# Kernel optimization log

Hardware: AMD Instinct MI355X
Metric: run time of the kernel (lower is better)

Reference implementation:

```python
import jax, jax.numpy as jnp
import numpy as np

K = 5          # kernel_size per dim
B = 100        # batch size (hard-coded in source)
GRID = 28
NUM_FIRST_FC = 49  # adjs[2].size(0) = 7*7


def spline_conv(x, edge_index, pseudo, W, root, bias):
    """Degree-1 open B-spline graph conv (SplineGCN).
    x: [N, Cin]; edge_index: [2, E] (src, dst); pseudo: [E, 2] in [0,1];
    W: [K*K, Cin, Cout]; root: [Cin, Cout]; bias: [Cout].
    out_i = mean_{j->i} sum_taps b_tap(u_ij) * (x_j @ W[k_tap]) + x_i @ root + bias
    """
    N = x.shape[0]
    src, dst = edge_index[0], edge_index[1]
    pos = pseudo * (K - 1)                     # open spline: scale to [0, K-1]
    kf = jnp.floor(pos)
    frac = pos - kf                            # [E, 2]
    k0 = kf.astype(jnp.int32)
    k1 = jnp.minimum(k0 + 1, K - 1)
    # Precompute x @ W[k] for all 25 kernel indices: [N, K*K, Cout]
    y = jnp.einsum('ni,kio->nko', x, W)
    fx, fy = frac[:, 0], frac[:, 1]
    taps = [
        (k0[:, 0], k0[:, 1], (1 - fx) * (1 - fy)),
        (k0[:, 0], k1[:, 1], (1 - fx) * fy),
        (k1[:, 0], k0[:, 1], fx * (1 - fy)),
        (k1[:, 0], k1[:, 1], fx * fy),
    ]
    msg = jnp.zeros((src.shape[0], W.shape[2]), dtype=x.dtype)
    for ax, ay, w in taps:
        msg = msg + w[:, None] * y[src, ax * K + ay]   # gather [E, Cout]
    agg = jax.ops.segment_sum(msg, dst, num_segments=N)
    deg = jax.ops.segment_sum(jnp.ones_like(msg[:, 0]), dst, num_segments=N)
    return agg / jnp.maximum(deg, 1.0)[:, None] + x @ root + bias


def max_pool2(x):  # x: [b, H, W, C] -> [b, H/2, W/2, C] (same math as NCHW pool)
    b, h, w, c = x.shape
    return x.reshape(b, h // 2, 2, w // 2, 2, c).max(axis=(2, 4))


def setup_inputs() -> dict:
    key = jax.random.key(0)
    ks = jax.random.split(key, 16)
    N0, N1 = B * GRID * GRID, B * (GRID // 2) * (GRID // 2)
    E0, E1 = N0 * 8, N1 * 8
    s = 0.1
    return {
        'x': jax.random.normal(ks[0], (N0, 1), dtype=jnp.float32),
        'pseudo0': jax.random.uniform(ks[1], (E0, 2), dtype=jnp.float32),
        'pseudo1': jax.random.uniform(ks[2], (E1, 2), dtype=jnp.float32),
        'W1': jax.random.normal(ks[3], (K * K, 1, 32), dtype=jnp.float32) * s,
        'root1': jax.random.normal(ks[4], (1, 32), dtype=jnp.float32) * s,
        'b1': jnp.zeros((32,), dtype=jnp.float32),
        'W2': jax.random.normal(ks[5], (K * K, 32, 64), dtype=jnp.float32) * s,
        'root2': jax.random.normal(ks[6], (32, 64), dtype=jnp.float32) * s,
        'b2': jnp.zeros((64,), dtype=jnp.float32),
        'fc1_w': jax.random.normal(ks[7], (NUM_FIRST_FC * 64, 512), dtype=jnp.float32) * 0.02,
        'fc1_b': jnp.zeros((512,), dtype=jnp.float32),
        'fc2_w': jax.random.normal(ks[8], (512, 10), dtype=jnp.float32) * 0.02,
        'fc2_b': jnp.zeros((10,), dtype=jnp.float32),
        'edge_index0': jax.random.randint(ks[9], (2, E0), 0, N0, dtype=jnp.int32),
        'edge_index1': jax.random.randint(ks[10], (2, E1), 0, N1, dtype=jnp.int32),
    }


def reference(x, pseudo0, pseudo1, W1, root1, b1, W2, root2, b2,
              fc1_w, fc1_b, fc2_w, fc2_b, edge_index0, edge_index1):
    elu = jax.nn.elu
    # conv1 on 28x28 grid graph
    h = elu(spline_conv(x, edge_index0, pseudo0, W1, root1, b1))   # [B*784, 32]
    h = h.reshape(-1, GRID, GRID, 32)                              # [B, 28, 28, 32]
    h = max_pool2(h)                                               # [B, 14, 14, 32]
    h = h.reshape(-1, 32)                                          # [B*196, 32]
    # conv2 on 14x14 grid graph
    h = elu(spline_conv(h, edge_index1, pseudo1, W2, root2, b2))   # [B*196, 64]
    # faithful replication of the source's reshapes: (B*196) rows -> (B/4, 28, 28, 64)
    h = h.reshape(-1, GRID, GRID, 64)                              # [25, 28, 28, 64]
    h = max_pool2(h)                                               # [25, 14, 14, 64]
    h = h.reshape(-1, NUM_FIRST_FC * 64)                           # [100, 3136]
    h = elu(h @ fc1_w + fc1_b)
    # F.dropout with training=False (eval) is identity
    h = elu(h @ fc2_w + fc2_b)
    return jax.nn.log_softmax(h, axis=-1)
```

## Files before the change

kernel.cpp:

```cpp
#include <hip/hip_runtime.h>
#include <hip/hip_bf16.h>

#define KK 5
constexpr int N0 = 78400;
constexpr int E0 = 627200;
constexpr int N1 = 19600;
constexpr int E1 = 156800;
constexpr int C1 = 32, C2 = 64;
constexpr int BSZ = 100;
constexpr int FC1_IN = 3136, FC1_OUT = 512;
constexpr int NKEYS = 98000;
constexpr int NCOARSE = 383;
constexpr int CAPB = 2400;
constexpr int KEXT = 832;
constexpr int ULS = 836;
constexpr int UBS = 856;
constexpr int CH2 = 160;

typedef __attribute__((ext_vector_type(8))) short bf16x8;
typedef __attribute__((ext_vector_type(4))) float f32x4;

__device__ __forceinline__ unsigned short f2bf(float f) {
    union { float f; unsigned u; } v; v.f = f;
    unsigned u = v.u;
    unsigned r = (u + 0x7FFF + ((u >> 16) & 1)) >> 16;
    return (unsigned short)r;
}

__device__ __forceinline__ void taps4(float px, float py,
                                      int& a00, int& a01, int& a10, int& a11,
                                      float& fx, float& fy) {
    float kfx = floorf(px), kfy = floorf(py);
    fx = px - kfx; fy = py - kfy;
    int k0x = min(max((int)kfx, 0), KK - 1);
    int k0y = min(max((int)kfy, 0), KK - 1);
    int k1x = min(k0x + 1, KK - 1), k1y = min(k0y + 1, KK - 1);
    a00 = k0x * KK + k0y; a01 = k0x * KK + k1y;
    a10 = k1x * KK + k0y; a11 = k1x * KK + k1y;
}

__global__ void coarse_bin(const int* __restrict__ ei0, const int* __restrict__ ei1,
                           int* __restrict__ gcur, int* __restrict__ pk) {
    __shared__ int hist[NCOARSE];
    __shared__ int gbase[NCOARSE];
    int t = threadIdx.x;
    for (int i = t; i < NCOARSE; i += 512) hist[i] = 0;
    __syncthreads();
    int e0b = blockIdx.x * 4096;
    int ids[8], keys[8], rnk[8];
#pragma unroll
    for (int j = 0; j < 8; j++) {
        int e = e0b + t + j * 512;
        int gk = -1, id = 0;
        if (e < E0) { gk = ei0[E0 + e]; id = e; }
        else if (e < E0 + E1) { int el = e - E0; gk = N0 + ei1[E1 + el]; id = el; }
        ids[j] = id; keys[j] = gk;
    }
#pragma unroll
    for (int j = 0; j < 8; j++)
        if (keys[j] >= 0) rnk[j] = atomicAdd(&hist[keys[j] >> 8], 1);
    __syncthreads();
    for (int i = t; i < NCOARSE; i += 512)
        gbase[i] = hist[i] ? atomicAdd(&gcur[i], hist[i]) : 0;
    __syncthreads();
#pragma unroll
    for (int j = 0; j < 8; j++) {
        if (keys[j] >= 0) {
            int b = keys[j] >> 8;
            int p = gbase[b] + rnk[j];
            if (p < CAPB) pk[b * CAPB + p] = ids[j] | ((keys[j] & 255) << 20);
        }
    }
}

__global__ void tiny_scan(const int* __restrict__ gcur, int* __restrict__ db,
                          int* __restrict__ off) {
    __shared__ int tmp[NCOARSE];
    int t = threadIdx.x;
    if (t < NCOARSE) tmp[t] = min(gcur[t], CAPB);
    __syncthreads();
    if (t == 0) {
        int s = 0;
        for (int i = 0; i < NCOARSE; i++) { int c = tmp[i]; tmp[i] = s; s += c; }
    }
    __syncthreads();
    if (t < NCOARSE) db[t] = tmp[t];
    if (t == 0) off[NKEYS] = E0 + E1;
}

__global__ void fine_sort(const int* __restrict__ pk, const int* __restrict__ gcur,
                          const int* __restrict__ db,
                          int* __restrict__ idxx, int* __restrict__ off) {
    __shared__ int ent[CAPB];
    __shared__ int rnk[CAPB];
    __shared__ int h2[256];
    __shared__ int sc[256];
    int b = blockIdx.x, t = threadIdx.x;
    int cb = min(gcur[b], CAPB);
    int base = db[b];
    h2[t] = 0;
    __syncthreads();
    for (int i = t; i < cb; i += 256) {
        int v = pk[b * CAPB + i];
        ent[i] = v;
        rnk[i] = atomicAdd(&h2[(v >> 20) & 255], 1);
    }
    __syncthreads();
    int v0 = h2[t];
    sc[t] = v0;
    __syncthreads();
    for (int d = 1; d < 256; d <<= 1) {
        int add = (t >= d) ? sc[t - d] : 0;
        __syncthreads();
        sc[t] += add;
        __syncthreads();
    }
    int excl = sc[t] - v0;
    __syncthreads();
    sc[t] = excl;
    __syncthreads();
    int n = (b << 8) + t;
    if (n < NKEYS) off[n] = base + excl;
    for (int i = t; i < cb; i += 256) {
        int v = ent[i];
        idxx[base + sc[(v >> 20) & 255] + rnk[i]] = v & 0xFFFFF;
    }
}

__global__ __launch_bounds__(256, 5)
void conv1_fused(const int* __restrict__ idxx, const int* __restrict__ off,
                 const float* __restrict__ x, const int* __restrict__ ei0,
                 const float* __restrict__ ps0, const float* __restrict__ W1,
                 const float* __restrict__ root, const float* __restrict__ bias,
                 float* __restrict__ h1) {
    __shared__ float S4[256 * 25];
    __shared__ float Sr[64 * 25];
    int t = threadIdx.x;
    int nb = blockIdx.x * 64;
    int q = t & 3, nl = t >> 2;
    int n = nb + nl;
    float* sp = S4 + t * 25;
#pragma unroll
    for (int a = 0; a < 25; a++) sp[a] = 0.f;
    int e0 = off[n], e1 = off[n + 1];
    for (int p = e0 + q; p < e1; p += 4) {
        int e = idxx[p];
        int src = ei0[e];
        int a00, a01, a10, a11; float fx, fy;
        taps4(ps0[2 * e] * (KK - 1), ps0[2 * e + 1] * (KK - 1),
              a00, a01, a10, a11, fx, fy);
        float xv = x[src];
        float gx = 1.f - fx, gy = 1.f - fy;
        sp[a00] += gx * gy * xv; sp[a01] += gx * fy * xv;
        sp[a10] += fx * gy * xv; sp[a11] += fx * fy * xv;
    }
    __syncthreads();
    for (int idx2 = t; idx2 < 64 * 25; idx2 += 256) {
        int n2 = idx2 / 25, a = idx2 - n2 * 25;
        Sr[idx2] = S4[(n2 * 4 + 0) * 25 + a] + S4[(n2 * 4 + 1) * 25 + a] +
                   S4[(n2 * 4 + 2) * 25 + a] + S4[(n2 * 4 + 3) * 25 + a];
    }
    __syncthreads();
    int o = t & 31, ng = t >> 5;
    float w1c[25];
#pragma unroll
    for (int a = 0; a < 25; a++) w1c[a] = W1[a * C1 + o];
    float ro = root[o], bo = bias[o];
    for (int j = 0; j < 8; j++) {
        int nl2 = ng * 8 + j;
        int n2 = nb + nl2;
        float acc = 0.f;
#pragma unroll
        for (int a = 0; a < 25; a++) acc += Sr[nl2 * 25 + a] * w1c[a];
        float invd = 1.f / fmaxf((float)(off[n2 + 1] - off[n2]), 1.f);
        float v = acc * invd + x[n2] * ro + bo;
        h1[n2 * C1 + o] = v > 0.f ? v : expm1f(v);
    }
}

__global__ void pool1(const float* __restrict__ h1, float* __restrict__ p1) {
    int idx = blockIdx.x * blockDim.x + threadIdx.x;
    if (idx >= N1 * C1) return;
    int o = idx & 31; int t = idx >> 5;
    int c = t % 14; int r = (t / 14) % 14; int b = t / 196;
    const float* base = h1 + (((b * 28 + 2 * r) * 28 + 2 * c) * C1 + o);
    float m = fmaxf(fmaxf(base[0], base[C1]),
                    fmaxf(base[28 * C1], base[28 * C1 + C1]));
    p1[idx] = m;
}

__global__ void w2t_prep(const float* __restrict__ W2, const float* __restrict__ root2,
                         unsigned short* __restrict__ w2t) {
    int idx = blockIdx.x * blockDim.x + threadIdx.x;
    if (idx >= 64 * KEXT) return;
    int o = idx / KEXT, k = idx - o * KEXT;
    float v = (k < 800) ? W2[k * 64 + o] : root2[(k - 800) * 64 + o];
    w2t[idx] = f2bf(v);
}

__global__ void wt1_prep(const float* __restrict__ w, unsigned short* __restrict__ wt1) {
    __shared__ unsigned short tile[64 * 66];
    int t = threadIdx.x;
    int k0 = blockIdx.x * 64, j0 = blockIdx.y * 64;
    int jj = t & 63, ks = t >> 6;
    for (int kk = ks; kk < 64; kk += 4)
        tile[kk * 66 + jj] = f2bf(w[(k0 + kk) * FC1_OUT + j0 + jj]);
    __syncthreads();
    int kk = t & 63, js = t >> 6;
    for (int j2 = js; j2 < 64; j2 += 4)
        wt1[(j0 + j2) * FC1_IN + k0 + kk] = tile[kk * 66 + j2];
}

__global__ __launch_bounds__(256, 5)
void conv2_fused(const float* __restrict__ p1, const int* __restrict__ idxx,
                 const int* __restrict__ off, const int* __restrict__ ei1,
                 const float* __restrict__ ps1,
                 const unsigned short* __restrict__ w2t,
                 const float* __restrict__ b2, float* __restrict__ h2) {
    __shared__ float Ul[8 * ULS];
    __shared__ int   es[CH2];
    __shared__ int   et[CH2];
    __shared__ float efx[CH2], efy[CH2];
    unsigned short* Ub = (unsigned short*)Ul;
    int t = threadIdx.x;
    int nb = blockIdx.x * 8;
    int i = t & 31, g = t >> 5;
    float* up = Ul + g * ULS;
#pragma unroll
    for (int a = 0; a < 25; a++) up[a * 32 + i] = 0.f;
    up[800 + i] = p1[(nb + g) * C1 + i];
    int e0 = off[N0 + nb], e1 = off[N0 + nb + 8];
    int my0 = off[N0 + nb + g], my1 = off[N0 + nb + g + 1];
    for (int base = e0; base < e1; base += CH2) {
        int nE = min(e1 - base, CH2);
        __syncthreads();
        for (int j = t; j < nE; j += 256) {
            int e = idxx[base + j];
            es[j] = ei1[e];
            int a00, a01, a10, a11; float fx, fy;
            taps4(ps1[2 * e] * (KK - 1), ps1[2 * e + 1] * (KK - 1),
                  a00, a01, a10, a11, fx, fy);
            et[j] = a00 | (a01 << 5) | (a10 << 10) | (a11 << 15);
            efx[j] = fx; efy[j] = fy;
        }
        __syncthreads();
        int r0 = max(my0 - base, 0);
        int r1 = min(my1 - base, nE);
#pragma unroll 2
        for (int j = r0; j < r1; j++) {
            int src = es[j]; int m = et[j];
            float fx = efx[j], fy = efy[j];
            float xv = p1[src * C1 + i];
            float gx = 1.f - fx, gy = 1.f - fy;
            up[(m & 31) * 32 + i]         += gx * gy * xv;
            up[((m >> 5) & 31) * 32 + i]  += gx * fy * xv;
            up[((m >> 10) & 31) * 32 + i] += fx * gy * xv;
            up[((m >> 15) & 31) * 32 + i] += fx * fy * xv;
        }
    }
    __syncthreads();
    {
        int g2 = t >> 5, ks = (t & 31) * 26;
        int dgc = off[N0 + nb + g2 + 1] - off[N0 + nb + g2];
        float invd = 1.f / fmaxf((float)dgc, 1.f);
        const float* srcp = Ul + g2 * ULS + ks;
        float rv[26];
#pragma unroll
        for (int j = 0; j < 26; j++) {
            float v = srcp[j];
            rv[j] = (ks + j < 800) ? v * invd : v;
        }
        __syncthreads();
        unsigned* dstp = (unsigned*)(Ub + g2 * UBS + ks);
#pragma unroll
        for (int j = 0; j < 13; j++) {
            unsigned lo = f2bf(rv[2 * j]), hi = f2bf(rv[2 * j + 1]);
            dstp[j] = lo | (hi << 16);
        }
    }
    __syncthreads();
    int wv = t >> 6, lane = t & 63, quad = lane >> 4, lrow = lane & 15;
    f32x4 acc = {0.f, 0.f, 0.f, 0.f};
    int nodeA = lrow & 7;
    const unsigned short* bbase = w2t + (wv * 16 + lrow) * KEXT;
    const unsigned short* abase = Ub + nodeA * UBS;
#pragma unroll
    for (int kc = 0; kc < 26; kc++) {
        bf16x8 a = *(const bf16x8*)(abase + kc * 32 + quad * 8);
        bf16x8 b = *(const bf16x8*)(bbase + kc * 32 + quad * 8);
        acc = __builtin_amdgcn_mfma_f32_16x16x32_bf16(a, b, acc, 0, 0, 0);
    }
    if (quad < 2) {
        int o = wv * 16 + lrow;
        float bo = b2[o];
#pragma unroll
        for (int r = 0; r < 4; r++) {
            int node = quad * 4 + r;
            float v = acc[r] + bo;
            v = v > 0.f ? v : expm1f(v);
            h2[(nb + node) * C2 + o] = v;
        }
    }
}

__global__ void pool2b(const float* __restrict__ h2, unsigned short* __restrict__ p2b) {
    int idx = blockIdx.x * blockDim.x + threadIdx.x;
    if (idx >= 112 * FC1_IN) return;
    if (idx >= 100 * FC1_IN) { p2b[idx] = 0; return; }
    int o = idx & 63; int t2 = idx >> 6;
    int c = t2 % 14; int r = (t2 / 14) % 14; int b = t2 / 196;
    const float* base = h2 + (((b * 28 + 2 * r) * 28 + 2 * c) * C2 + o);
    float m = fmaxf(fmaxf(base[0], base[C2]),
                    fmaxf(base[28 * C2], base[28 * C2 + C2]));
    p2b[idx] = f2bf(m);
}

__global__ void gemm_fc1(const unsigned short* __restrict__ p2b,
                         const unsigned short* __restrict__ wt1,
                         float* __restrict__ z1p) {
    constexpr int AS = 232;
    __shared__ unsigned short as_[16 * AS];
    int t = threadIdx.x;
    int jt = blockIdx.x, mt = blockIdx.y, kz = blockIdx.z;
    int wv = t >> 6, lane = t & 63, quad = lane >> 4, lrow = lane & 15;
    int m0 = mt * 16;
    int kbase = kz * 1568;
    const unsigned short* bbase = wt1 + (jt * 64 + wv * 16 + lrow) * FC1_IN + kbase;
    f32x4 acc = {0.f, 0.f, 0.f, 0.f};
    for (int ch = 0; ch < 7; ch++) {
        __syncthreads();
        for (int slot = t; slot < 448; slot += 256) {
            int r = slot / 28, c = slot - (slot / 28) * 28;
            *(uint4*)(as_ + r * AS + c * 8) =
                *(const uint4*)(p2b + (m0 + r) * FC1_IN + kbase + ch * 224 + c * 8);
        }
        __syncthreads();
        const unsigned short* ab = as_ + lrow * AS;
        const unsigned short* bb = bbase + ch * 224;
#pragma unroll
        for (int kk = 0; kk < 7; kk++) {
            bf16x8 a = *(const bf16x8*)(ab + kk * 32 + quad * 8);
            bf16x8 b = *(const bf16x8*)(bb + kk * 32 + quad * 8);
            acc = __builtin_amdgcn_mfma_f32_16x16x32_bf16(a, b, acc, 0, 0, 0);
        }
    }
    int n = jt * 64 + wv * 16 + lrow;
#pragma unroll
    for (int r = 0; r < 4; r++) {
        int m = m0 + quad * 4 + r;
        z1p[kz * (112 * FC1_OUT) + m * FC1_OUT + n] = acc[r];
    }
}

__global__ void fc2_lsm(const float* __restrict__ z1p, const float* __restrict__ fc1b,
                        const float* __restrict__ w, const float* __restrict__ fc2b,
                        float* __restrict__ out) {
    int b = blockIdx.x;
    int t = threadIdx.x;
    int wv = t >> 6;
    int lane = t & 63;
    float acc = 0.f;
#pragma unroll
    for (int m = 0; m < 8; m++) {
        int k = lane * 8 + m;
        float xv = fc1b[k] + z1p[b * FC1_OUT + k] + z1p[112 * FC1_OUT + b * FC1_OUT + k];
        xv = xv > 0.f ? xv : expm1f(xv);
        acc += xv * w[k * 10 + wv];
    }
#pragma unroll
    for (int off = 32; off > 0; off >>= 1) acc += __shfl_down(acc, off);
    __shared__ float zs[10];
    if (lane == 0) {
        float z = acc + fc2b[wv];
        zs[wv] = z > 0.f ? z : expm1f(z);
    }
    __syncthreads();
    if (t < 10) {
        float m = -1e30f;
        for (int jj = 0; jj < 10; jj++) m = fmaxf(m, zs[jj]);
        float s = 0.f;
        for (int jj = 0; jj < 10; jj++) s += expf(zs[jj] - m);
        out[b * 10 + t] = zs[t] - m - logf(s);
    }
}

extern "C" void kernel_launch(void* const* d_in, const int* in_sizes, int n_in,
                              void* d_out, int out_size, void* d_ws, size_t ws_size,
                              hipStream_t stream) {
    const float* x     = (const float*)d_in[0];
    const float* ps0   = (const float*)d_in[1];
    const float* ps1   = (const float*)d_in[2];
    const float* W1    = (const float*)d_in[3];
    const float* root1 = (const float*)d_in[4];
    const float* b1    = (const float*)d_in[5];
    const float* W2    = (const float*)d_in[6];
    const float* root2 = (const float*)d_in[7];
    const float* b2v   = (const float*)d_in[8];
    const float* fc1w  = (const float*)d_in[9];
    const float* fc1b  = (const float*)d_in[10];
    const float* fc2w  = (const float*)d_in[11];
    const float* fc2b  = (const float*)d_in[12];
    const int*   ei0   = (const int*)d_in[13];
    const int*   ei1   = (const int*)d_in[14];

    float* ws = (float*)d_ws;
    int* gcur  = (int*)ws;
    int* db    = (int*)(ws + 384);
    int* off   = (int*)(ws + 768);
    int* pk    = (int*)(ws + 98772);
    int* idxx  = (int*)(ws + 1017972);
    float* h1  = ws + 1801972;
    float* p1  = ws + 4310772;
    float* h2  = ws + 4937972;
    unsigned short* p2b = (unsigned short*)(ws + 6192372);
    float* z1p = ws + 6367988;
    unsigned short* w2t = (unsigned short*)(ws + 6482676);
    unsigned short* wt1 = (unsigned short*)(ws + 6509300);

    hipMemsetAsync(gcur, 0, (size_t)NCOARSE * sizeof(int), stream);

    coarse_bin<<<(E0 + E1 + 4095) / 4096, 512, 0, stream>>>(ei0, ei1, gcur, pk);
    tiny_scan<<<1, 512, 0, stream>>>(gcur, db, off);
    fine_sort<<<NCOARSE, 256, 0, stream>>>(pk, gcur, db, idxx, off);
    w2t_prep<<<(64 * KEXT + 255) / 256, 256, 0, stream>>>(W2, root2, w2t);
    wt1_prep<<<dim3(49, 8), 256, 0, stream>>>(fc1w, wt1);
    conv1_fused<<<N0 / 64, 256, 0, stream>>>(idxx, off, x, ei0, ps0,
                                             W1, root1, b1, h1);
    pool1<<<(N1 * C1 + 255) / 256, 256, 0, stream>>>(h1, p1);
    conv2_fused<<<N1 / 8, 256, 0, stream>>>(p1, idxx, off, ei1, ps1, w2t, b2v, h2);
    pool2b<<<(112 * FC1_IN + 255) / 256, 256, 0, stream>>>(h2, p2b);
    gemm_fc1<<<dim3(8, 7, 2), 256, 0, stream>>>(p2b, wt1, z1p);
    fc2_lsm<<<BSZ, 640, 0, stream>>>(z1p, fc1b, fc2w, fc2b, (float*)d_out);
}
```

Baseline: 225.4 us.

## Fuse conv1 with max-pool, stage edges in LDS, merge weight-prep kernels

Conv1 now processes two image rows (56 nodes) per block, so the 2x2 max-pool is done in shared memory and the full-resolution h1 is never written to global memory. Each block stages its edge metadata (tap indices, fractions, gathered x values) in shared memory with coalesced loads, replacing per-lane scattered loads. The two weight-prep kernels are merged into one launch, and the conv2 edge loop is made uniform across the wavefront using a shuffle-based max trip count. Costs include fewer resident blocks per CU (launch bounds drop from 5 to 4), idle lanes in conv1 (224 of 256 threads active), and extra shuffle and predication in conv2.

```diff
diff --git a/kernel.cpp b/kernel.cpp
--- a/kernel.cpp
+++ b/kernel.cpp
@@ -16,6 +16,7 @@
 constexpr int ULS = 836;
 constexpr int UBS = 856;
 constexpr int CH2 = 160;
+constexpr int CH1 = 640;
 
 typedef __attribute__((ext_vector_type(8))) short bf16x8;
 typedef __attribute__((ext_vector_type(4))) float f32x4;
@@ -127,78 +128,101 @@
     }
 }
 
-__global__ __launch_bounds__(256, 5)
-void conv1_fused(const int* __restrict__ idxx, const int* __restrict__ off,
-                 const float* __restrict__ x, const int* __restrict__ ei0,
-                 const float* __restrict__ ps0, const float* __restrict__ W1,
-                 const float* __restrict__ root, const float* __restrict__ bias,
-                 float* __restrict__ h1) {
-    __shared__ float S4[256 * 25];
-    __shared__ float Sr[64 * 25];
-    int t = threadIdx.x;
-    int nb = blockIdx.x * 64;
+__global__ __launch_bounds__(256, 4)
+void conv1_pool(const int* __restrict__ idxx, const int* __restrict__ off,
+                const float* __restrict__ x, const int* __restrict__ ei0,
+                const float* __restrict__ ps0, const float* __restrict__ W1,
+                const float* __restrict__ root, const float* __restrict__ bias,
+                float* __restrict__ p1) {
+    __shared__ float S4[224 * 25];
+    __shared__ float Sr[56 * 25];
+    __shared__ float exv[CH1], efx[CH1], efy[CH1];
+    __shared__ int   emt[CH1];
+    float* h1t = S4;
+    int t = threadIdx.x;
+    int bb = blockIdx.x;
+    int n0 = bb * 56;
     int q = t & 3, nl = t >> 2;
-    int n = nb + nl;
-    float* sp = S4 + t * 25;
-#pragma unroll
-    for (int a = 0; a < 25; a++) sp[a] = 0.f;
-    int e0 = off[n], e1 = off[n + 1];
-    for (int p = e0 + q; p < e1; p += 4) {
-        int e = idxx[p];
-        int src = ei0[e];
-        int a00, a01, a10, a11; float fx, fy;
-        taps4(ps0[2 * e] * (KK - 1), ps0[2 * e + 1] * (KK - 1),
-              a00, a01, a10, a11, fx, fy);
-        float xv = x[src];
-        float gx = 1.f - fx, gy = 1.f - fy;
-        sp[a00] += gx * gy * xv; sp[a01] += gx * fy * xv;
-        sp[a10] += fx * gy * xv; sp[a11] += fx * fy * xv;
-    }
-    __syncthreads();
-    for (int idx2 = t; idx2 < 64 * 25; idx2 += 256) {
-        int n2 = idx2 / 25, a = idx2 - n2 * 25;
-        Sr[idx2] = S4[(n2 * 4 + 0) * 25 + a] + S4[(n2 * 4 + 1) * 25 + a] +
-                   S4[(n2 * 4 + 2) * 25 + a] + S4[(n2 * 4 + 3) * 25 + a];
-    }
-    __syncthreads();
-    int o = t & 31, ng = t >> 5;
-    float w1c[25];
-#pragma unroll
-    for (int a = 0; a < 25; a++) w1c[a] = W1[a * C1 + o];
-    float ro = root[o], bo = bias[o];
-    for (int j = 0; j < 8; j++) {
-        int nl2 = ng * 8 + j;
-        int n2 = nb + nl2;
-        float acc = 0.f;
-#pragma unroll
-        for (int a = 0; a < 25; a++) acc += Sr[nl2 * 25 + a] * w1c[a];
-        float invd = 1.f / fmaxf((float)(off[n2 + 1] - off[n2]), 1.f);
-        float v = acc * invd + x[n2] * ro + bo;
-        h1[n2 * C1 + o] = v > 0.f ? v : expm1f(v);
-    }
-}
-
-__global__ void pool1(const float* __restrict__ h1, float* __restrict__ p1) {
-    int idx = blockIdx.x * blockDim.x + threadIdx.x;
-    if (idx >= N1 * C1) return;
-    int o = idx & 31; int t = idx >> 5;
-    int c = t % 14; int r = (t / 14) % 14; int b = t / 196;
-    const float* base = h1 + (((b * 28 + 2 * r) * 28 + 2 * c) * C1 + o);
-    float m = fmaxf(fmaxf(base[0], base[C1]),
-                    fmaxf(base[28 * C1], base[28 * C1 + C1]));
-    p1[idx] = m;
-}
-
-__global__ void w2t_prep(const float* __restrict__ W2, const float* __restrict__ root2,
-                         unsigned short* __restrict__ w2t) {
-    int idx = blockIdx.x * blockDim.x + threadIdx.x;
-    if (idx >= 64 * KEXT) return;
-    int o = idx / KEXT, k = idx - o * KEXT;
-    float v = (k < 800) ? W2[k * 64 + o] : root2[(k - 800) * 64 + o];
-    w2t[idx] = f2bf(v);
-}
-
-__global__ void wt1_prep(const float* __restrict__ w, unsigned short* __restrict__ wt1) {
+    bool actN = nl < 56;
+    int n = n0 + (actN ? nl : 0);
+    float* sp = S4 + (actN ? (nl * 4 + q) : 0) * 25;
+    for (int i = t; i < 224 * 25; i += 256) S4[i] = 0.f;
+    int e0 = off[n0], e1 = off[n0 + 56];
+    int my0 = off[n], my1 = off[n + 1];
+    for (int base = e0; base < e1; base += CH1) {
+        int nE = min(e1 - base, CH1);
+        __syncthreads();
+        for (int j = t; j < nE; j += 256) {
+            int e = idxx[base + j];
+            int src = ei0[e];
+            int a00, a01, a10, a11; float fx, fy;
+            taps4(ps0[2 * e] * (KK - 1), ps0[2 * e + 1] * (KK - 1),
+                  a00, a01, a10, a11, fx, fy);
+            emt[j] = a00 | (a01 << 5) | (a10 << 10) | (a11 << 15);
+            efx[j] = fx; efy[j] = fy;
+            exv[j] = x[src];
+        }
+        __syncthreads();
+        if (actN) {
+            int r0 = max(my0 - base, 0), r1 = min(my1 - base, nE);
+            for (int p = r0 + q; p < r1; p += 4) {
+                float xv = exv[p]; int m = emt[p];
+                float fx = efx[p], fy = efy[p];
+                float gx = 1.f - fx, gy = 1.f - fy;
+                sp[m & 31]         += gx * gy * xv;
+                sp[(m >> 5) & 31]  += gx * fy * xv;
+                sp[(m >> 10) & 31] += fx * gy * xv;
+                sp[(m >> 15) & 31] += fx * fy * xv;
+            }
+        }
+    }
+    __syncthreads();
+    for (int i2 = t; i2 < 56 * 25; i2 += 256) {
+        int n2 = i2 / 25, a = i2 - n2 * 25;
+        Sr[i2] = S4[(n2 * 4 + 0) * 25 + a] + S4[(n2 * 4 + 1) * 25 + a] +
+                 S4[(n2 * 4 + 2) * 25 + a] + S4[(n2 * 4 + 3) * 25 + a];
+    }
+    __syncthreads();
+    {
+        int o = t & 31, ng = t >> 5;
+        float w1c[25];
+#pragma unroll
+        for (int a = 0; a < 25; a++) w1c[a] = W1[a * C1 + o];
+        float ro = root[o], bo = bias[o];
+        for (int j2 = 0; j2 < 7; j2++) {
+            int nl2 = ng * 7 + j2;
+            int n2 = n0 + nl2;
+            float acc = 0.f;
+#pragma unroll
+            for (int a = 0; a < 25; a++) acc += Sr[nl2 * 25 + a] * w1c[a];
+            float invd = 1.f / fmaxf((float)(off[n2 + 1] - off[n2]), 1.f);
+            float v = acc * invd + x[n2] * ro + bo;
+            h1t[nl2 * 32 + o] = v > 0.f ? v : expm1f(v);
+        }
+    }
+    __syncthreads();
+    for (int i2 = t; i2 < 448; i2 += 256) {
+        int o2 = i2 & 31, pc = i2 >> 5;
+        float m0 = h1t[(2 * pc) * 32 + o2],      m1 = h1t[(2 * pc + 1) * 32 + o2];
+        float m2 = h1t[(28 + 2 * pc) * 32 + o2], m3 = h1t[(28 + 2 * pc + 1) * 32 + o2];
+        p1[(bb * 14 + pc) * C1 + o2] = fmaxf(fmaxf(m0, m1), fmaxf(m2, m3));
+    }
+}
+
+__global__ void prep_weights(const float* __restrict__ w, const float* __restrict__ W2,
+                             const float* __restrict__ root2,
+                             unsigned short* __restrict__ wt1,
+                             unsigned short* __restrict__ w2t) {
+    if (blockIdx.x == 49) {
+        int base = blockIdx.y * 6656;
+        for (int i = threadIdx.x; i < 6656; i += 256) {
+            int idx = base + i;
+            int o = idx / KEXT, k = idx - o * KEXT;
+            float v = (k < 800) ? W2[k * 64 + o] : root2[(k - 800) * 64 + o];
+            w2t[idx] = f2bf(v);
+        }
+        return;
+    }
     __shared__ unsigned short tile[64 * 66];
     int t = threadIdx.x;
     int k0 = blockIdx.x * 64, j0 = blockIdx.y * 64;
@@ -246,16 +270,23 @@
         __syncthreads();
         int r0 = max(my0 - base, 0);
         int r1 = min(my1 - base, nE);
+        int myT = max(r1 - r0, 0);
+        int m64 = max(myT, __shfl_xor(myT, 32));
 #pragma unroll 2
-        for (int j = r0; j < r1; j++) {
-            int src = es[j]; int m = et[j];
-            float fx = efx[j], fy = efy[j];
+        for (int jj = 0; jj < m64; jj++) {
+            int j = r0 + jj;
+            bool act = j < r1;
+            int ji = act ? j : 0;
+            int src = es[ji]; int m = et[ji];
+            float fx = efx[ji], fy = efy[ji];
             float xv = p1[src * C1 + i];
-            float gx = 1.f - fx, gy = 1.f - fy;
-            up[(m & 31) * 32 + i]         += gx * gy * xv;
-            up[((m >> 5) & 31) * 32 + i]  += gx * fy * xv;
-            up[((m >> 10) & 31) * 32 + i] += fx * gy * xv;
-            up[((m >> 15) & 31) * 32 + i] += fx * fy * xv;
+            if (act) {
+                float gx = 1.f - fx, gy = 1.f - fy;
+                up[(m & 31) * 32 + i]         += gx * gy * xv;
+                up[((m >> 5) & 31) * 32 + i]  += gx * fy * xv;
+                up[((m >> 10) & 31) * 32 + i] += fx * gy * xv;
+                up[((m >> 15) & 31) * 32 + i] += fx * fy * xv;
+            }
         }
     }
     __syncthreads();
@@ -409,24 +440,21 @@
     int* off   = (int*)(ws + 768);
     int* pk    = (int*)(ws + 98772);
     int* idxx  = (int*)(ws + 1017972);
-    float* h1  = ws + 1801972;
-    float* p1  = ws + 4310772;
-    float* h2  = ws + 4937972;
-    unsigned short* p2b = (unsigned short*)(ws + 6192372);
-    float* z1p = ws + 6367988;
-    unsigned short* w2t = (unsigned short*)(ws + 6482676);
-    unsigned short* wt1 = (unsigned short*)(ws + 6509300);
+    float* p1  = ws + 1801972;
+    float* h2  = ws + 2429172;
+    unsigned short* p2b = (unsigned short*)(ws + 3683572);
+    float* z1p = ws + 3859188;
+    unsigned short* w2t = (unsigned short*)(ws + 3973876);
+    unsigned short* wt1 = (unsigned short*)(ws + 4000500);
 
     hipMemsetAsync(gcur, 0, (size_t)NCOARSE * sizeof(int), stream);
 
     coarse_bin<<<(E0 + E1 + 4095) / 4096, 512, 0, stream>>>(ei0, ei1, gcur, pk);
     tiny_scan<<<1, 512, 0, stream>>>(gcur, db, off);
     fine_sort<<<NCOARSE, 256, 0, stream>>>(pk, gcur, db, idxx, off);
-    w2t_prep<<<(64 * KEXT + 255) / 256, 256, 0, stream>>>(W2, root2, w2t);
-    wt1_prep<<<dim3(49, 8), 256, 0, stream>>>(fc1w, wt1);
-    conv1_fused<<<N0 / 64, 256, 0, stream>>>(idxx, off, x, ei0, ps0,
-                                             W1, root1, b1, h1);
-    pool1<<<(N1 * C1 + 255) / 256, 256, 0, stream>>>(h1, p1);
+    prep_weights<<<dim3(50, 8), 256, 0, stream>>>(fc1w, W2, root2, wt1, w2t);
+    conv1_pool<<<1400, 256, 0, stream>>>(idxx, off, x, ei0, ps0,
+                                         W1, root1, b1, p1);
     conv2_fused<<<N1 / 8, 256, 0, stream>>>(p1, idxx, off, ei1, ps1, w2t, b2v, h2);
     pool2b<<<(112 * FC1_IN + 255) / 256, 256, 0, stream>>>(h2, p2b);
     gemm_fc1<<<dim3(8, 7, 2), 256, 0, stream>>>(p2b, wt1, z1p);
```

Result: no change. 228.0 us (+1.2%).
